# Kernel optimization log

Hardware: AMD Instinct MI355X
Metric: run time of the kernel (lower is better)

Reference implementation:

```python
import jax, jax.numpy as jnp
import numpy as np

NUM_HEADS = 16
HEAD_DIM = 128
QUERY_DIM = 2048
SCALE = HEAD_DIM ** -0.5


def setup_inputs() -> dict:
    key = jax.random.key(0)
    ks = jax.random.split(key, 11)
    B, L, D = 2, 2048, QUERY_DIM
    HD = NUM_HEADS * HEAD_DIM
    s = 0.02
    return {
        "x_q": jax.random.normal(ks[0], (B, L, D), jnp.float32),
        "x_k": jax.random.normal(ks[1], (B, L, D), jnp.float32),
        "x_v": jax.random.normal(ks[2], (B, L, D), jnp.float32),
        "Wq": jax.random.normal(ks[3], (D, HD), jnp.float32) * s,
        "bq": jnp.zeros((HD,), jnp.float32),
        "Wk": jax.random.normal(ks[4], (D, HD), jnp.float32) * s,
        "bk": jnp.zeros((HD,), jnp.float32),
        "Wv": jax.random.normal(ks[5], (D, HD), jnp.float32) * s,
        "bv": jnp.zeros((HD,), jnp.float32),
        "Wo": jax.random.normal(ks[6], (HD, D), jnp.float32) * s,
        "bo": jnp.zeros((D,), jnp.float32),
    }


def _split_heads(x):  # [b, l, h*d] -> [b, h, l, d]
    b, l, _ = x.shape
    return x.reshape(b, l, NUM_HEADS, HEAD_DIM).transpose(0, 2, 1, 3)


def reference(x_q, x_k, x_v, Wq, bq, Wk, bk, Wv, bv, Wo, bo):
    # Note: the torch module constructs norm_q/norm_k but NEVER applies them in forward.
    q = _split_heads(x_q @ Wq + bq)  # [b, h, l, d]
    k = _split_heads(x_k @ Wk + bk)
    v = _split_heads(x_v @ Wv + bv)
    scores = jnp.einsum("bhid,bhjd->bhij", q, k) * SCALE
    probs = jax.nn.softmax(scores, axis=-1)
    o = jnp.einsum("bhij,bhjd->bhid", probs, v)  # [b, h, l, d]
    b, h, l, d = o.shape
    o = o.transpose(0, 2, 1, 3).reshape(b, l, h * d)
    return o @ Wo + bo
```

## Files before the change

kernel.cpp:

```cpp
#include <hip/hip_runtime.h>


typedef _Float16 f16;
typedef __attribute__((ext_vector_type(8))) _Float16 f16x8;
typedef __attribute__((ext_vector_type(4))) _Float16 f16x4;
typedef __attribute__((ext_vector_type(4))) float f32x4;
typedef __attribute__((ext_vector_type(4))) unsigned int u32x4;

#define QSCALE (0.08838834764831845f * 1.4426950408889634f)
#define SWZ3(r) (((r) & 3) | (((r) >> 1) & 4))
#define SWZV(r) ((r) & 7)
#define SWZG(r) (((r) >> 1) & 3)

static __device__ __forceinline__ void gload16(void* lds, const void* g) {
  __builtin_amdgcn_global_load_lds(
      (__attribute__((address_space(1))) void*)g,
      (__attribute__((address_space(3))) void*)lds, 16, 0, 0);
}

__global__ __launch_bounds__(256) void cvt_x_kernel(
    const float* __restrict__ x0, const float* __restrict__ x1,
    const float* __restrict__ x2, f16* __restrict__ out) {
  const float* x = blockIdx.z == 0 ? x0 : (blockIdx.z == 1 ? x1 : x2);
  f16* o = out + (size_t)blockIdx.z * 8388608;
  size_t i = ((size_t)blockIdx.x * 256 + threadIdx.x) * 8;
  f32x4 a = *(const f32x4*)(x + i);
  f32x4 b = *(const f32x4*)(x + i + 4);
  f16x8 r;
  r[0] = (f16)a[0]; r[1] = (f16)a[1]; r[2] = (f16)a[2]; r[3] = (f16)a[3];
  r[4] = (f16)b[0]; r[5] = (f16)b[1]; r[6] = (f16)b[2]; r[7] = (f16)b[3];
  *(f16x8*)(o + i) = r;
}

__global__ __launch_bounds__(256) void cvt_w_kernel(
    const float* __restrict__ w0, const float* __restrict__ w1,
    const float* __restrict__ w2, const float* __restrict__ w3,
    f16* __restrict__ out) {
  const float* W = blockIdx.z == 0 ? w0 : blockIdx.z == 1 ? w1
                 : blockIdx.z == 2 ? w2 : w3;
  f16* WT = out + (size_t)blockIdx.z * 4194304;
  __shared__ f16 tile[64][68];
  const int tx = threadIdx.x & 15, ty = threadIdx.x >> 4;
  const int k0 = blockIdx.y * 64, n0 = blockIdx.x * 64;
#pragma unroll
  for (int i = 0; i < 4; ++i) {
    int r = ty + i * 16;
    f32x4 v = *(const f32x4*)(W + (size_t)(k0 + r) * 2048 + n0 + tx * 4);
    tile[r][tx * 4 + 0] = (f16)v[0]; tile[r][tx * 4 + 1] = (f16)v[1];
    tile[r][tx * 4 + 2] = (f16)v[2]; tile[r][tx * 4 + 3] = (f16)v[3];
  }
  __syncthreads();
#pragma unroll
  for (int i = 0; i < 4; ++i) {
    int n = ty + i * 16;
    f16x4 o;
    o[0] = tile[tx * 4 + 0][n]; o[1] = tile[tx * 4 + 1][n];
    o[2] = tile[tx * 4 + 2][n]; o[3] = tile[tx * 4 + 3][n];
    *(f16x4*)(WT + (size_t)(n0 + n) * 2048 + k0 + tx * 4) = o;
  }
}

template <int MODE>
__global__ __launch_bounds__(512, 4) void gemm128_kernel(
    const f16* __restrict__ Abase, const f16* __restrict__ Btbase,
    void* __restrict__ Obase, const float* __restrict__ b0,
    const float* __restrict__ b1, const float* __restrict__ b2) {
  constexpr int BN = MODE == 0 ? 256 : 128;
  constexpr int NJ = MODE == 0 ? 4 : 2;
  constexpr int NSPAN = MODE == 0 ? 64 : 32;
  constexpr int BLOADS = MODE == 0 ? 2 : 1;
  constexpr int BUFSZ = 8192 + BN * 64;
  const int lid = blockIdx.x;
  int bn, bm, z;
  if (MODE == 0) {
    const int logi = (lid & 7) * 96 + (lid >> 3);
    bn = logi & 7; bm = (logi >> 3) & 31; z = logi >> 8;
  } else {
    const int logi = (lid & 7) * 64 + (lid >> 3);
    bn = logi & 15; bm = logi >> 4; z = 0;
  }
  const f16* A  = Abase  + (size_t)z * 8388608;
  const f16* Bt = Btbase + (size_t)z * 4194304;
  const float* bias = z == 0 ? b0 : (z == 1 ? b1 : b2);
  const float qsc = (MODE == 0 && z == 0) ? QSCALE : 1.0f;
  const int tid = threadIdx.x, lane = tid & 63, w = tid >> 6;
  const int wm = w >> 2, wn = w & 3;
  const int l15 = lane & 15, lg = lane >> 4;
  __shared__ alignas(16) char smb[2 * BUFSZ];

  f32x4 acc[4][NJ];
#pragma unroll
  for (int i = 0; i < 4; ++i)
#pragma unroll
    for (int j = 0; j < NJ; ++j) acc[i][j] = (f32x4)0.f;

#define GSTAGE(KT, C_)                                                        \
  {                                                                           \
    char* Ab_ = smb + (C_) * BUFSZ;                                           \
    char* Bb_ = Ab_ + 8192;                                                   \
    {                                                                         \
      int L = tid * 16;                                                       \
      int row = L >> 6, pcol = L & 63;                                        \
      int scol = pcol ^ (SWZG(row) << 4);                                     \
      gload16(Ab_ + L,                                                        \
              (const char*)A + ((size_t)(bm * 128 + row) * 2048 + (KT) * 32) * 2 + scol); \
    }                                                                         \
    _Pragma("unroll") for (int p = 0; p < BLOADS; ++p) {                      \
      int L = p * 8192 + tid * 16;                                            \
      int row = L >> 6, pcol = L & 63;                                        \
      int scol = pcol ^ (SWZG(row) << 4);                                     \
      gload16(Bb_ + L,                                                        \
              (const char*)Bt + ((size_t)(bn * BN + row) * 2048 + (KT) * 32) * 2 + scol); \
    }                                                                         \
  }

  GSTAGE(0, 0);
#pragma unroll 1
  for (int kt = 0; kt < 64; ++kt) {
    const int c = kt & 1;
    if (kt < 63) {
      GSTAGE(kt + 1, c ^ 1);
      if constexpr (MODE == 0)
        asm volatile("s_waitcnt vmcnt(3)" ::: "memory");
      else
        asm volatile("s_waitcnt vmcnt(2)" ::: "memory");
    } else {
      asm volatile("s_waitcnt vmcnt(0)" ::: "memory");
    }
    __builtin_amdgcn_s_barrier();

    const char* Ab = smb + c * BUFSZ;
    const char* Bb = Ab + 8192;
    f16x8 af[4], bf[NJ];
#pragma unroll
    for (int i = 0; i < 4; ++i) {
      int row = wm * 64 + i * 16 + l15;
      af[i] = *(const f16x8*)(Ab + row * 64 + ((lg * 16) ^ (SWZG(row) << 4)));
    }
#pragma unroll
    for (int j = 0; j < NJ; ++j) {
      int row = wn * NSPAN + j * 16 + l15;
      bf[j] = *(const f16x8*)(Bb + row * 64 + ((lg * 16) ^ (SWZG(row) << 4)));
    }
    asm volatile("s_waitcnt lgkmcnt(0)" ::: "memory");
    __builtin_amdgcn_sched_barrier(0);
    __builtin_amdgcn_s_setprio(1);
#pragma unroll
    for (int i = 0; i < 4; ++i)
#pragma unroll
      for (int j = 0; j < NJ; ++j)
        acc[i][j] = __builtin_amdgcn_mfma_f32_16x16x32_f16(af[i], bf[j], acc[i][j], 0, 0, 0);
    __builtin_amdgcn_s_setprio(0);
    __builtin_amdgcn_sched_barrier(0);
    __builtin_amdgcn_s_barrier();
  }

  if (MODE == 0) {
    f16* Oz = (f16*)Obase + (size_t)z * 8388608;
#pragma unroll
    for (int i = 0; i < 4; ++i)
#pragma unroll
      for (int j = 0; j < NJ; ++j) {
        int col = bn * BN + wn * NSPAN + j * 16 + l15;
        int h = col >> 7, d = col & 127;
        float bv = bias[col];
#pragma unroll
        for (int r = 0; r < 4; ++r) {
          int rowg = bm * 128 + wm * 64 + i * 16 + lg * 4 + r;
          int b_ = rowg >> 11, lpos = rowg & 2047;
          Oz[(size_t)(b_ * 16 + h) * 262144 + (size_t)lpos * 128 + d] =
              (f16)((acc[i][j][r] + bv) * qsc);
        }
      }
  } else {
    float* Out = (float*)Obase;
#pragma unroll
    for (int i = 0; i < 4; ++i)
#pragma unroll
      for (int j = 0; j < NJ; ++j) {
        int col = bn * BN + wn * NSPAN + j * 16 + l15;
        float bv = bias[col];
#pragma unroll
        for (int r = 0; r < 4; ++r) {
          int rowg = bm * 128 + wm * 64 + i * 16 + lg * 4 + r;
          Out[(size_t)rowg * 2048 + col] = acc[i][j][r] + bv;
        }
      }
  }
#undef GSTAGE
}

__global__ __launch_bounds__(256) void tr_v_kernel(const f16* __restrict__ v,
                                                   f16* __restrict__ vtout) {
  const int bh = blockIdx.z;
  const f16* V = v + (size_t)bh * 262144;
  f16* VT = vtout + (size_t)bh * 262144;
  __shared__ f16 tile[64][68];
  const int tx = threadIdx.x & 15, ty = threadIdx.x >> 4;
  const int l0 = blockIdx.x * 64, d0 = blockIdx.y * 64;
#pragma unroll
  for (int i = 0; i < 4; ++i) {
    int r = ty + i * 16;
    f16x4 val = *(const f16x4*)(V + (size_t)(l0 + r) * 128 + d0 + tx * 4);
    tile[r][tx * 4 + 0] = val[0]; tile[r][tx * 4 + 1] = val[1];
    tile[r][tx * 4 + 2] = val[2]; tile[r][tx * 4 + 3] = val[3];
  }
  __syncthreads();
#pragma unroll
  for (int i = 0; i < 4; ++i) {
    int d = ty + i * 16;
    f16x4 o;
    o[0] = tile[tx * 4 + 0][d]; o[1] = tile[tx * 4 + 1][d];
    o[2] = tile[tx * 4 + 2][d]; o[3] = tile[tx * 4 + 3][d];
    *(f16x4*)(VT + (size_t)(d0 + d) * 2048 + l0 + tx * 4) = o;
  }
}

__global__ __launch_bounds__(512, 4) void attn_kernel(
    const f16* __restrict__ q, const f16* __restrict__ k,
    const f16* __restrict__ vt, f16* __restrict__ o) {
  const int orig = blockIdx.y * 16 + blockIdx.x;
  const int swz = (orig & 7) * 64 + (orig >> 3);
  const int qt = swz & 15, bh = swz >> 4;
  const int tid = threadIdx.x, lane = tid & 63, w = tid >> 6;
  const int l15 = lane & 15, lg = lane >> 4;
  const f16* Qb = q + (size_t)bh * 262144 + (size_t)qt * 128 * 128;
  const char* Kb = (const char*)(k + (size_t)bh * 262144);
  const char* Vtb = (const char*)(vt + (size_t)bh * 262144);
  __shared__ alignas(16) char sm[65536];

  f16x8 qf[4];
#pragma unroll
  for (int ks = 0; ks < 4; ++ks)
    qf[ks] = *(const f16x8*)(Qb + (w * 16 + l15) * 128 + ks * 32 + lg * 8);

  f32x4 oacc[8];
#pragma unroll
  for (int df = 0; df < 8; ++df) oacc[df] = (f32x4)0.f;
  float mrow = -1e30f, ps = 0.f;
  const int rA = ((l15 >> 2) << 3) + (l15 & 3);

#define STAGE(T, B)                                                          \
  {                                                                          \
    char* Ks_ = sm + (B) * 32768;                                            \
    char* Vs_ = Ks_ + 16384;                                                 \
    _Pragma("unroll") for (int i = 0; i < 2; ++i) {                          \
      int c = i * 8 + w;                                                     \
      int phys = c * 1024 + lane * 16;                                       \
      {                                                                      \
        int row = phys >> 8, pcol = phys & 255;                              \
        int lcol = pcol ^ (SWZ3(row) << 4);                                  \
        gload16(Ks_ + c * 1024, Kb + (size_t)((T) * 64 + row) * 256 + lcol); \
      }                                                                      \
      {                                                                      \
        int row = phys >> 7, pcol = phys & 127;                              \
        int lcol = pcol ^ (SWZV(row) << 4);                                  \
        gload16(Vs_ + c * 1024, Vtb + (size_t)row * 4096 + (T) * 128 + lcol);\
      }                                                                      \
    }                                                                        \
  }

  STAGE(0, 0);
  int cur = 0;
  for (int t = 0; t < 32; ++t) {
    __syncthreads();
    if (t < 31) STAGE(t + 1, cur ^ 1);
    const char* Ks = sm + cur * 32768;
    const char* Vs = Ks + 16384;

    f32x4 s[4];
#pragma unroll
    for (int nf = 0; nf < 4; ++nf) s[nf] = (f32x4)0.f;
    __builtin_amdgcn_s_setprio(1);
#pragma unroll
    for (int ks = 0; ks < 4; ++ks) {
      f16x8 kf[4];
#pragma unroll
      for (int nf = 0; nf < 4; ++nf) {
        int row = ((nf & 1) << 5) + ((nf >> 1) << 2) + rA;
        int colb = (ks * 64 + lg * 16) ^ (SWZ3(row) << 4);
        kf[nf] = *(const f16x8*)(Ks + row * 256 + colb);
      }
#pragma unroll
      for (int nf = 0; nf < 4; ++nf)
        s[nf] = __builtin_amdgcn_mfma_f32_16x16x32_f16(kf[nf], qf[ks], s[nf], 0, 0, 0);
    }
    __builtin_amdgcn_s_setprio(0);

    unsigned int pk[2][4];
    {
      float m0 = fmaxf(fmaxf(s[0][0], s[0][1]), fmaxf(s[0][2], s[0][3]));
      float m1 = fmaxf(fmaxf(s[1][0], s[1][1]), fmaxf(s[1][2], s[1][3]));
      float m2 = fmaxf(fmaxf(s[2][0], s[2][1]), fmaxf(s[2][2], s[2][3]));
      float m3 = fmaxf(fmaxf(s[3][0], s[3][1]), fmaxf(s[3][2], s[3][3]));
      float mx = fmaxf(fmaxf(m0, m1), fmaxf(m2, m3));
      mx = fmaxf(mx, __shfl_xor(mx, 16));
      mx = fmaxf(mx, __shfl_xor(mx, 32));
      if (!__all(mx <= mrow + 8.f)) {
        float mnew = fmaxf(mrow, mx);
        float sc = exp2f(mrow - mnew);
        mrow = mnew;
        ps *= sc;
#pragma unroll
        for (int r = 0; r < 4; ++r) {
          float scr = __shfl(sc, (lane & 48) | (lg * 4 + r));
#pragma unroll
          for (int df = 0; df < 8; ++df) oacc[df][r] *= scr;
        }
      }
      float m = mrow;
      float psum = 0.f;
#pragma unroll
      for (int nf = 0; nf < 4; ++nf)
#pragma unroll
        for (int h = 0; h < 2; ++h) {
          float p0 = exp2f(s[nf][2 * h] - m);
          float p1 = exp2f(s[nf][2 * h + 1] - m);
          psum += p0 + p1;
          pk[nf & 1][(nf >> 1) * 2 + h] =
              __builtin_bit_cast(unsigned int, __builtin_amdgcn_cvt_pkrtz(p0, p1));
        }
      ps += psum;
    }

    __builtin_amdgcn_s_setprio(1);
#pragma unroll
    for (int kvs = 0; kvs < 2; ++kvs) {
      f16x8 pa = __builtin_bit_cast(f16x8, *(const u32x4*)pk[kvs]);
#pragma unroll
      for (int df = 0; df < 8; ++df) {
        int row = df * 16 + l15;
        int colb = (kvs * 64 + lg * 16) ^ (SWZV(row) << 4);
        f16x8 vb = *(const f16x8*)(Vs + row * 128 + colb);
        oacc[df] = __builtin_amdgcn_mfma_f32_16x16x32_f16(pa, vb, oacc[df], 0, 0, 0);
      }
    }
    __builtin_amdgcn_s_setprio(0);
    cur ^= 1;
  }

  const int b_ = bh >> 4, h_ = bh & 15;
  f16* Ob = o + (size_t)b_ * 4194304 + (size_t)qt * 128 * 2048 + h_ * 128;
  float lr = ps;
  lr += __shfl_xor(lr, 16);
  lr += __shfl_xor(lr, 32);
  float inv = 1.f / lr;
#pragma unroll
  for (int r = 0; r < 4; ++r) {
    float invr = __shfl(inv, (lane & 48) | (lg * 4 + r));
    int rl = w * 16 + lg * 4 + r;
#pragma unroll
    for (int df = 0; df < 8; ++df)
      Ob[(size_t)rl * 2048 + df * 16 + l15] = (f16)(oacc[df][r] * invr);
  }
#undef STAGE
}

extern "C" void kernel_launch(void* const* d_in, const int* in_sizes, int n_in,
                              void* d_out, int out_size, void* d_ws, size_t ws_size,
                              hipStream_t stream) {
  const float* xq = (const float*)d_in[0];
  const float* xk = (const float*)d_in[1];
  const float* xv = (const float*)d_in[2];
  const float* Wq = (const float*)d_in[3];
  const float* bq = (const float*)d_in[4];
  const float* Wk = (const float*)d_in[5];
  const float* bk = (const float*)d_in[6];
  const float* Wv = (const float*)d_in[7];
  const float* bv = (const float*)d_in[8];
  const float* Wo = (const float*)d_in[9];
  const float* bo = (const float*)d_in[10];

  char* ws = (char*)d_ws;
  f16* xh   = (f16*)(ws);
  f16* wt   = (f16*)(ws + 50331648);
  f16* qkv  = (f16*)(ws + 83886080);
  f16* vtb  = (f16*)(ws);
  f16* oatt = (f16*)(ws + 16777216);
  float* outp = (float*)d_out;

  hipLaunchKernelGGL(cvt_x_kernel, dim3(4096, 1, 3), dim3(256), 0, stream,
                     xq, xk, xv, xh);
  hipLaunchKernelGGL(cvt_w_kernel, dim3(32, 32, 4), dim3(256), 0, stream,
                     Wq, Wk, Wv, Wo, wt);
  hipLaunchKernelGGL((gemm128_kernel<0>), dim3(768), dim3(512), 0, stream,
                     xh, wt, (void*)qkv, bq, bk, bv);
  hipLaunchKernelGGL(tr_v_kernel, dim3(32, 2, 32), dim3(256), 0, stream,
                     qkv + (size_t)2 * 8388608, vtb);
  hipLaunchKernelGGL(attn_kernel, dim3(16, 32), dim3(512), 0, stream,
                     qkv, qkv + (size_t)8388608, vtb, oatt);
  hipLaunchKernelGGL((gemm128_kernel<1>), dim3(512), dim3(512), 0, stream,
                     oatt, wt + (size_t)3 * 4194304, (void*)outp, bo, bo, bo);
}
```

Before: 296.8 us.

## Give each QKV GEMM wave a 128x64 tile with 256-thread blocks

```diff
diff --git a/kernel.cpp b/kernel.cpp
--- a/kernel.cpp
+++ b/kernel.cpp
@@ -60,43 +60,133 @@
   }
 }
 
-template <int MODE>
-__global__ __launch_bounds__(512, 4) void gemm128_kernel(
+__global__ __launch_bounds__(256, 3) void gemm_qkv_kernel(
     const f16* __restrict__ Abase, const f16* __restrict__ Btbase,
-    void* __restrict__ Obase, const float* __restrict__ b0,
+    f16* __restrict__ Obase, const float* __restrict__ b0,
     const float* __restrict__ b1, const float* __restrict__ b2) {
-  constexpr int BN = MODE == 0 ? 256 : 128;
-  constexpr int NJ = MODE == 0 ? 4 : 2;
-  constexpr int NSPAN = MODE == 0 ? 64 : 32;
-  constexpr int BLOADS = MODE == 0 ? 2 : 1;
-  constexpr int BUFSZ = 8192 + BN * 64;
   const int lid = blockIdx.x;
-  int bn, bm, z;
-  if (MODE == 0) {
-    const int logi = (lid & 7) * 96 + (lid >> 3);
-    bn = logi & 7; bm = (logi >> 3) & 31; z = logi >> 8;
-  } else {
-    const int logi = (lid & 7) * 64 + (lid >> 3);
-    bn = logi & 15; bm = logi >> 4; z = 0;
-  }
+  const int logi = (lid & 7) * 96 + (lid >> 3);
+  const int bn = logi & 7, bm = (logi >> 3) & 31, z = logi >> 8;
   const f16* A  = Abase  + (size_t)z * 8388608;
   const f16* Bt = Btbase + (size_t)z * 4194304;
+  f16* Oz = Obase + (size_t)z * 8388608;
   const float* bias = z == 0 ? b0 : (z == 1 ? b1 : b2);
-  const float qsc = (MODE == 0 && z == 0) ? QSCALE : 1.0f;
+  const float qsc = z == 0 ? QSCALE : 1.0f;
+  const int tid = threadIdx.x, lane = tid & 63, w = tid >> 6;
+  const int l15 = lane & 15, lg = lane >> 4;
+  __shared__ alignas(16) char smb[49152];
+
+  f32x4 acc[8][4];
+#pragma unroll
+  for (int i = 0; i < 8; ++i)
+#pragma unroll
+    for (int j = 0; j < 4; ++j) acc[i][j] = (f32x4)0.f;
+
+#define GSTAGE(KT, C_)                                                        \
+  {                                                                           \
+    char* Ab_ = smb + (C_) * 24576;                                           \
+    char* Bb_ = Ab_ + 8192;                                                   \
+    _Pragma("unroll") for (int p = 0; p < 2; ++p) {                           \
+      int L = p * 4096 + tid * 16;                                            \
+      int row = L >> 6, pcol = L & 63;                                        \
+      int scol = pcol ^ (SWZG(row) << 4);                                     \
+      gload16(Ab_ + L,                                                        \
+              (const char*)A + ((size_t)(bm * 128 + row) * 2048 + (KT) * 32) * 2 + scol); \
+    }                                                                         \
+    _Pragma("unroll") for (int p = 0; p < 4; ++p) {                           \
+      int L = p * 4096 + tid * 16;                                            \
+      int row = L >> 6, pcol = L & 63;                                        \
+      int scol = pcol ^ (SWZG(row) << 4);                                     \
+      gload16(Bb_ + L,                                                        \
+              (const char*)Bt + ((size_t)(bn * 256 + row) * 2048 + (KT) * 32) * 2 + scol); \
+    }                                                                         \
+  }
+
+  GSTAGE(0, 0);
+#pragma unroll 1
+  for (int kt = 0; kt < 64; ++kt) {
+    const int c = kt & 1;
+    if (kt < 63) {
+      GSTAGE(kt + 1, c ^ 1);
+      asm volatile("s_waitcnt vmcnt(6)" ::: "memory");
+    } else {
+      asm volatile("s_waitcnt vmcnt(0)" ::: "memory");
+    }
+    __builtin_amdgcn_s_barrier();
+
+    const char* Ab = smb + c * 24576;
+    const char* Bb = Ab + 8192;
+    f16x8 bf[4], af[4];
+#pragma unroll
+    for (int j = 0; j < 4; ++j) {
+      int row = w * 64 + j * 16 + l15;
+      bf[j] = *(const f16x8*)(Bb + row * 64 + ((lg * 16) ^ (SWZG(row) << 4)));
+    }
+#pragma unroll
+    for (int i = 0; i < 4; ++i) {
+      int row = i * 16 + l15;
+      af[i] = *(const f16x8*)(Ab + row * 64 + ((lg * 16) ^ (SWZG(row) << 4)));
+    }
+    __builtin_amdgcn_s_setprio(1);
+#pragma unroll
+    for (int i = 0; i < 4; ++i)
+#pragma unroll
+      for (int j = 0; j < 4; ++j)
+        acc[i][j] = __builtin_amdgcn_mfma_f32_16x16x32_f16(af[i], bf[j], acc[i][j], 0, 0, 0);
+    __builtin_amdgcn_s_setprio(0);
+#pragma unroll
+    for (int i = 0; i < 4; ++i) {
+      int row = (4 + i) * 16 + l15;
+      af[i] = *(const f16x8*)(Ab + row * 64 + ((lg * 16) ^ (SWZG(row) << 4)));
+    }
+    __builtin_amdgcn_s_setprio(1);
+#pragma unroll
+    for (int i = 0; i < 4; ++i)
+#pragma unroll
+      for (int j = 0; j < 4; ++j)
+        acc[4 + i][j] = __builtin_amdgcn_mfma_f32_16x16x32_f16(af[i], bf[j], acc[4 + i][j], 0, 0, 0);
+    __builtin_amdgcn_s_setprio(0);
+    __builtin_amdgcn_s_barrier();
+  }
+
+#pragma unroll
+  for (int i = 0; i < 8; ++i)
+#pragma unroll
+    for (int j = 0; j < 4; ++j) {
+      int col = bn * 256 + w * 64 + j * 16 + l15;
+      int h = col >> 7, d = col & 127;
+      float bv = bias[col];
+#pragma unroll
+      for (int r = 0; r < 4; ++r) {
+        int rowg = bm * 128 + i * 16 + lg * 4 + r;
+        int b_ = rowg >> 11, lpos = rowg & 2047;
+        Oz[(size_t)(b_ * 16 + h) * 262144 + (size_t)lpos * 128 + d] =
+            (f16)((acc[i][j][r] + bv) * qsc);
+      }
+    }
+#undef GSTAGE
+}
+
+__global__ __launch_bounds__(512, 4) void gemm_out_kernel(
+    const f16* __restrict__ A, const f16* __restrict__ Bt,
+    float* __restrict__ Out, const float* __restrict__ bias) {
+  const int lid = blockIdx.x;
+  const int logi = (lid & 7) * 64 + (lid >> 3);
+  const int bn = logi & 15, bm = logi >> 4;
   const int tid = threadIdx.x, lane = tid & 63, w = tid >> 6;
   const int wm = w >> 2, wn = w & 3;
   const int l15 = lane & 15, lg = lane >> 4;
-  __shared__ alignas(16) char smb[2 * BUFSZ];
-
-  f32x4 acc[4][NJ];
+  __shared__ alignas(16) char smb[32768];
+
+  f32x4 acc[4][2];
 #pragma unroll
   for (int i = 0; i < 4; ++i)
 #pragma unroll
-    for (int j = 0; j < NJ; ++j) acc[i][j] = (f32x4)0.f;
+    for (int j = 0; j < 2; ++j) acc[i][j] = (f32x4)0.f;
 
 #define GSTAGE(KT, C_)                                                        \
   {                                                                           \
-    char* Ab_ = smb + (C_) * BUFSZ;                                           \
+    char* Ab_ = smb + (C_) * 16384;                                           \
     char* Bb_ = Ab_ + 8192;                                                   \
     {                                                                         \
       int L = tid * 16;                                                       \
@@ -105,12 +195,12 @@
       gload16(Ab_ + L,                                                        \
               (const char*)A + ((size_t)(bm * 128 + row) * 2048 + (KT) * 32) * 2 + scol); \
     }                                                                         \
-    _Pragma("unroll") for (int p = 0; p < BLOADS; ++p) {                      \
-      int L = p * 8192 + tid * 16;                                            \
+    {                                                                         \
+      int L = tid * 16;                                                       \
       int row = L >> 6, pcol = L & 63;                                        \
       int scol = pcol ^ (SWZG(row) << 4);                                     \
       gload16(Bb_ + L,                                                        \
-              (const char*)Bt + ((size_t)(bn * BN + row) * 2048 + (KT) * 32) * 2 + scol); \
+              (const char*)Bt + ((size_t)(bn * 128 + row) * 2048 + (KT) * 32) * 2 + scol); \
     }                                                                         \
   }
 
@@ -120,26 +210,23 @@
     const int c = kt & 1;
     if (kt < 63) {
       GSTAGE(kt + 1, c ^ 1);
-      if constexpr (MODE == 0)
-        asm volatile("s_waitcnt vmcnt(3)" ::: "memory");
-      else
-        asm volatile("s_waitcnt vmcnt(2)" ::: "memory");
+      asm volatile("s_waitcnt vmcnt(2)" ::: "memory");
     } else {
       asm volatile("s_waitcnt vmcnt(0)" ::: "memory");
     }
     __builtin_amdgcn_s_barrier();
 
-    const char* Ab = smb + c * BUFSZ;
+    const char* Ab = smb + c * 16384;
     const char* Bb = Ab + 8192;
-    f16x8 af[4], bf[NJ];
+    f16x8 af[4], bf[2];
 #pragma unroll
     for (int i = 0; i < 4; ++i) {
       int row = wm * 64 + i * 16 + l15;
       af[i] = *(const f16x8*)(Ab + row * 64 + ((lg * 16) ^ (SWZG(row) << 4)));
     }
 #pragma unroll
-    for (int j = 0; j < NJ; ++j) {
-      int row = wn * NSPAN + j * 16 + l15;
+    for (int j = 0; j < 2; ++j) {
+      int row = wn * 32 + j * 16 + l15;
       bf[j] = *(const f16x8*)(Bb + row * 64 + ((lg * 16) ^ (SWZG(row) << 4)));
     }
     asm volatile("s_waitcnt lgkmcnt(0)" ::: "memory");
@@ -148,45 +235,25 @@
 #pragma unroll
     for (int i = 0; i < 4; ++i)
 #pragma unroll
-      for (int j = 0; j < NJ; ++j)
+      for (int j = 0; j < 2; ++j)
         acc[i][j] = __builtin_amdgcn_mfma_f32_16x16x32_f16(af[i], bf[j], acc[i][j], 0, 0, 0);
     __builtin_amdgcn_s_setprio(0);
     __builtin_amdgcn_sched_barrier(0);
     __builtin_amdgcn_s_barrier();
   }
 
-  if (MODE == 0) {
-    f16* Oz = (f16*)Obase + (size_t)z * 8388608;
-#pragma unroll
-    for (int i = 0; i < 4; ++i)
-#pragma unroll
-      for (int j = 0; j < NJ; ++j) {
-        int col = bn * BN + wn * NSPAN + j * 16 + l15;
-        int h = col >> 7, d = col & 127;
-        float bv = bias[col];
-#pragma unroll
-        for (int r = 0; r < 4; ++r) {
-          int rowg = bm * 128 + wm * 64 + i * 16 + lg * 4 + r;
-          int b_ = rowg >> 11, lpos = rowg & 2047;
-          Oz[(size_t)(b_ * 16 + h) * 262144 + (size_t)lpos * 128 + d] =
-              (f16)((acc[i][j][r] + bv) * qsc);
-        }
+#pragma unroll
+  for (int i = 0; i < 4; ++i)
+#pragma unroll
+    for (int j = 0; j < 2; ++j) {
+      int col = bn * 128 + wn * 32 + j * 16 + l15;
+      float bv = bias[col];
+#pragma unroll
+      for (int r = 0; r < 4; ++r) {
+        int rowg = bm * 128 + wm * 64 + i * 16 + lg * 4 + r;
+        Out[(size_t)rowg * 2048 + col] = acc[i][j][r] + bv;
       }
-  } else {
-    float* Out = (float*)Obase;
-#pragma unroll
-    for (int i = 0; i < 4; ++i)
-#pragma unroll
-      for (int j = 0; j < NJ; ++j) {
-        int col = bn * BN + wn * NSPAN + j * 16 + l15;
-        float bv = bias[col];
-#pragma unroll
-        for (int r = 0; r < 4; ++r) {
-          int rowg = bm * 128 + wm * 64 + i * 16 + lg * 4 + r;
-          Out[(size_t)rowg * 2048 + col] = acc[i][j][r] + bv;
-        }
-      }
-  }
+    }
 #undef GSTAGE
 }
 
@@ -383,12 +450,12 @@
                      xq, xk, xv, xh);
   hipLaunchKernelGGL(cvt_w_kernel, dim3(32, 32, 4), dim3(256), 0, stream,
                      Wq, Wk, Wv, Wo, wt);
-  hipLaunchKernelGGL((gemm128_kernel<0>), dim3(768), dim3(512), 0, stream,
-                     xh, wt, (void*)qkv, bq, bk, bv);
+  hipLaunchKernelGGL(gemm_qkv_kernel, dim3(768), dim3(256), 0, stream,
+                     xh, wt, qkv, bq, bk, bv);
   hipLaunchKernelGGL(tr_v_kernel, dim3(32, 2, 32), dim3(256), 0, stream,
                      qkv + (size_t)2 * 8388608, vtb);
   hipLaunchKernelGGL(attn_kernel, dim3(16, 32), dim3(512), 0, stream,
                      qkv, qkv + (size_t)8388608, vtb, oatt);
-  hipLaunchKernelGGL((gemm128_kernel<1>), dim3(512), dim3(512), 0, stream,
-                     oatt, wt + (size_t)3 * 4194304, (void*)outp, bo, bo, bo);
-}
+  hipLaunchKernelGGL(gemm_out_kernel, dim3(512), dim3(512), 0, stream,
+                     oatt, wt + (size_t)3 * 4194304, outp, bo);
+}
```

Result: slower. 328.2 us (+10.6%).
